# Optimization experiments

Measured on AMD Instinct MI355X. Metric: run time of the kernel, lower is better.

Reference implementation:

```python
import jax, jax.numpy as jnp
import numpy as np

T = 0.07
MOMENTUM = 0.5
B, D = 128, 128
N = 200000
K1 = 2048  # K + 1


def setup_inputs() -> dict:
    key = jax.random.key(0)
    ks = jax.random.split(key, 12)
    stdv = 1.0 / np.sqrt(D / 3.0)
    def bank(k):
        return jax.random.uniform(k, (N, D), dtype=jnp.float32) * (2 * stdv) - stdv
    l = jax.random.normal(ks[0], (B, D), dtype=jnp.float32)
    ab = jax.random.normal(ks[1], (B, D), dtype=jnp.float32)
    ori = jax.random.normal(ks[2], (B, D), dtype=jnp.float32)
    comp = jax.random.normal(ks[3], (B, D), dtype=jnp.float32)
    y = jax.random.randint(ks[4], (B,), 0, N, dtype=jnp.int32)
    idx = jax.random.randint(ks[5], (B, K1), 0, N, dtype=jnp.int32)
    idx = idx.at[:, 0].set(y)  # positive sample in slot 0
    return {
        'l': l, 'ab': ab, 'ori': ori, 'comp': comp, 'y': y, 'idx': idx,
        'memory_l': bank(ks[6]), 'memory_ab': bank(ks[7]),
        'memory_ori': bank(ks[8]), 'memory_comp': bank(ks[9]),
    }


def reference(l, ab, ori, comp, y, idx, memory_l, memory_ab, memory_ori, memory_comp):
    flat = idx.reshape(-1)
    # gather (B*K1, D) rows then fold back to (B, K1, D); weights are detached in torch
    w_l = jax.lax.stop_gradient(memory_l[flat]).reshape(B, K1, D)
    w_ab = jax.lax.stop_gradient(memory_ab[flat]).reshape(B, K1, D)
    w_ori = jax.lax.stop_gradient(memory_ori[flat]).reshape(B, K1, D)
    w_comp = jax.lax.stop_gradient(memory_comp[flat]).reshape(B, K1, D)

    dot = lambda w, v: jnp.einsum('bkd,bd->bk', w, v) / T  # use_softmax path
    out_ab_l = dot(w_l, ab)
    out_l_ori = dot(w_ori, l)
    out_ori_ab = dot(w_ab, ori)
    out_ab_comp = dot(w_comp, ab)
    out_l_comp = dot(w_comp, l)
    out_comp_ori = dot(w_ori, comp)
    outs = jnp.stack([out_l_ori, out_ab_l, out_ori_ab,
                      out_ab_comp, out_l_comp, out_comp_ori])[..., None]  # [6,B,K1,1]

    def ema_update(mem, v):
        pos = mem[y] * MOMENTUM + v * (1.0 - MOMENTUM)
        pos = pos / jnp.sqrt(jnp.sum(pos * pos, axis=1, keepdims=True))
        return mem.at[y].set(pos)

    return (outs,
            ema_update(memory_l, l),
            ema_update(memory_ab, ab),
            ema_update(memory_ori, ori),
            ema_update(memory_comp, comp))
```

## Files before the change

kernel.cpp:

```cpp
#include <hip/hip_runtime.h>

#define BB 128
#define DD 128
#define KK1 2048
#define NROWS 200000

static constexpr float INV_T = 1.0f / 0.07f;
static constexpr float MOM = 0.5f;

__global__ __launch_bounds__(256) void outs_kernel(
    const float* __restrict__ l, const float* __restrict__ ab,
    const float* __restrict__ ori, const float* __restrict__ comp,
    const int* __restrict__ idx,
    const float* __restrict__ ml, const float* __restrict__ mab,
    const float* __restrict__ mori, const float* __restrict__ mcomp,
    float* __restrict__ outs) {
  const int gid = blockIdx.x * blockDim.x + threadIdx.x;
  const int wave = gid >> 6;
  const int lane = threadIdx.x & 63;
  if (wave >= BB * KK1) return;
  const int b = wave >> 11;

  const int row = idx[wave];
  const size_t roff = (size_t)row * DD;

  const float2 wl    = ((const float2*)(ml    + roff))[lane];
  const float2 wab   = ((const float2*)(mab   + roff))[lane];
  const float2 wori  = ((const float2*)(mori  + roff))[lane];
  const float2 wcomp = ((const float2*)(mcomp + roff))[lane];

  const size_t voff = (size_t)b * DD;
  const float2 vl    = ((const float2*)(l    + voff))[lane];
  const float2 vab   = ((const float2*)(ab   + voff))[lane];
  const float2 vori  = ((const float2*)(ori  + voff))[lane];
  const float2 vcomp = ((const float2*)(comp + voff))[lane];

  float d0 = wori.x  * vl.x    + wori.y  * vl.y;
  float d1 = wl.x    * vab.x   + wl.y    * vab.y;
  float d2 = wab.x   * vori.x  + wab.y   * vori.y;
  float d3 = wcomp.x * vab.x   + wcomp.y * vab.y;
  float d4 = wcomp.x * vl.x    + wcomp.y * vl.y;
  float d5 = wori.x  * vcomp.x + wori.y  * vcomp.y;

#pragma unroll
  for (int off = 32; off > 0; off >>= 1) {
    d0 += __shfl_down(d0, off);
    d1 += __shfl_down(d1, off);
    d2 += __shfl_down(d2, off);
    d3 += __shfl_down(d3, off);
    d4 += __shfl_down(d4, off);
    d5 += __shfl_down(d5, off);
  }

  if (lane == 0) {
    const int BK = BB * KK1;
    outs[0 * BK + wave] = d0 * INV_T;
    outs[1 * BK + wave] = d1 * INV_T;
    outs[2 * BK + wave] = d2 * INV_T;
    outs[3 * BK + wave] = d3 * INV_T;
    outs[4 * BK + wave] = d4 * INV_T;
    outs[5 * BK + wave] = d5 * INV_T;
  }
}

__global__ __launch_bounds__(256) void copy_banks(
    const float4* __restrict__ s0, const float4* __restrict__ s1,
    const float4* __restrict__ s2, const float4* __restrict__ s3,
    float4* __restrict__ d0, float4* __restrict__ d1,
    float4* __restrict__ d2, float4* __restrict__ d3) {
  const int n = NROWS * DD / 4;
  const int stride = gridDim.x * blockDim.x;
  for (int i = blockIdx.x * blockDim.x + threadIdx.x; i < n; i += stride) {
    d0[i] = s0[i];
    d1[i] = s1[i];
    d2[i] = s2[i];
    d3[i] = s3[i];
  }
}

__global__ __launch_bounds__(64) void ema_kernel(
    const float* __restrict__ l, const float* __restrict__ ab,
    const float* __restrict__ ori, const float* __restrict__ comp,
    const int* __restrict__ y,
    const float* __restrict__ ml, const float* __restrict__ mab,
    const float* __restrict__ mori, const float* __restrict__ mcomp,
    float* __restrict__ ol, float* __restrict__ oab,
    float* __restrict__ oori, float* __restrict__ ocomp) {
  const int b = blockIdx.x;
  const int bank = blockIdx.y;
  const int row = y[b];
  for (int b2 = b + 1; b2 < BB; ++b2)
    if (y[b2] == row) return;

  const float* v;
  const float* mem;
  float* out;
  switch (bank) {
    case 0: v = l;    mem = ml;    out = ol;    break;
    case 1: v = ab;   mem = mab;   out = oab;   break;
    case 2: v = ori;  mem = mori;  out = oori;  break;
    default: v = comp; mem = mcomp; out = ocomp; break;
  }

  const int lane = threadIdx.x;
  const float2 m2 = ((const float2*)(mem + (size_t)row * DD))[lane];
  const float2 v2 = ((const float2*)(v + (size_t)b * DD))[lane];
  float2 p;
  p.x = m2.x * MOM + v2.x * (1.0f - MOM);
  p.y = m2.y * MOM + v2.y * (1.0f - MOM);

  float ss = p.x * p.x + p.y * p.y;
#pragma unroll
  for (int off = 32; off > 0; off >>= 1) ss += __shfl_down(ss, off);
  ss = __shfl(ss, 0);
  const float inv = 1.0f / sqrtf(ss);

  ((float2*)(out + (size_t)row * DD))[lane] = make_float2(p.x * inv, p.y * inv);
}

extern "C" void kernel_launch(void* const* d_in, const int* in_sizes, int n_in,
                              void* d_out, int out_size, void* d_ws, size_t ws_size,
                              hipStream_t stream) {
  const float* l     = (const float*)d_in[0];
  const float* ab    = (const float*)d_in[1];
  const float* ori   = (const float*)d_in[2];
  const float* comp  = (const float*)d_in[3];
  const int*   y     = (const int*)d_in[4];
  const int*   idx   = (const int*)d_in[5];
  const float* ml    = (const float*)d_in[6];
  const float* mab   = (const float*)d_in[7];
  const float* mori  = (const float*)d_in[8];
  const float* mcomp = (const float*)d_in[9];

  float* out = (float*)d_out;
  const size_t OUTS = (size_t)6 * BB * KK1;
  const size_t BANK = (size_t)NROWS * DD;
  float* o_outs  = out;
  float* o_ml    = out + OUTS;
  float* o_mab   = o_ml + BANK;
  float* o_mori  = o_mab + BANK;
  float* o_mcomp = o_mori + BANK;

  {
    const int waves = BB * KK1;
    const int blocks = waves / 4;
    outs_kernel<<<blocks, 256, 0, stream>>>(l, ab, ori, comp, idx,
                                            ml, mab, mori, mcomp, o_outs);
  }

  {
    copy_banks<<<4096, 256, 0, stream>>>(
        (const float4*)ml, (const float4*)mab, (const float4*)mori,
        (const float4*)mcomp, (float4*)o_ml, (float4*)o_mab,
        (float4*)o_mori, (float4*)o_mcomp);
  }

  {
    dim3 grid(BB, 4);
    ema_kernel<<<grid, 64, 0, stream>>>(l, ab, ori, comp, y,
                                        ml, mab, mori, mcomp,
                                        o_ml, o_mab, o_mori, o_mcomp);
  }
}
```

Before: 786.4 us.

## Fuse bank copy and gather-dot kernels into one interleaved launch

Merges the gather-dot kernel and the memory-bank copy kernel into a single launch. One of every five blocks does the bank copy and the other four compute the dot products, so the random-gather traffic and the streaming copy run at the same time instead of one after the other. The dot path now uses half-waves with float4 loads, two rows per wave, and xor shuffles over 32 lanes. The copy uses nontemporal stores to keep the output bank writes out of the cache. Interleaving the two kinds of block risks contention for bandwidth, and the block-index arithmetic must cover every row exactly.

```diff
diff --git a/kernel.cpp b/kernel.cpp
--- a/kernel.cpp
+++ b/kernel.cpp
@@ -8,73 +8,94 @@
 static constexpr float INV_T = 1.0f / 0.07f;
 static constexpr float MOM = 0.5f;
 
-__global__ __launch_bounds__(256) void outs_kernel(
+typedef float f4 __attribute__((ext_vector_type(4)));
+
+#define COPY_BLOCKS 8192
+#define OUTS_BLOCKS 32768
+#define TOTAL_BLOCKS (COPY_BLOCKS * 5)
+
+__global__ __launch_bounds__(256) void fused_kernel(
     const float* __restrict__ l, const float* __restrict__ ab,
     const float* __restrict__ ori, const float* __restrict__ comp,
     const int* __restrict__ idx,
     const float* __restrict__ ml, const float* __restrict__ mab,
     const float* __restrict__ mori, const float* __restrict__ mcomp,
-    float* __restrict__ outs) {
-  const int gid = blockIdx.x * blockDim.x + threadIdx.x;
-  const int wave = gid >> 6;
+    float* __restrict__ outs,
+    float* __restrict__ ol, float* __restrict__ oab,
+    float* __restrict__ oori, float* __restrict__ ocomp) {
+  const int bid = blockIdx.x;
+  const int q = bid / 5;
+  const int r = bid - q * 5;
+
+  if (r == 2) {
+    const int n = NROWS * DD / 4;
+    const int stride = COPY_BLOCKS * 256;
+    const f4* s0 = (const f4*)ml;
+    const f4* s1 = (const f4*)mab;
+    const f4* s2 = (const f4*)mori;
+    const f4* s3 = (const f4*)mcomp;
+    f4* d0 = (f4*)ol;
+    f4* d1 = (f4*)oab;
+    f4* d2 = (f4*)oori;
+    f4* d3 = (f4*)ocomp;
+    for (int i = q * 256 + threadIdx.x; i < n; i += stride) {
+      f4 a0 = s0[i];
+      f4 a1 = s1[i];
+      f4 a2 = s2[i];
+      f4 a3 = s3[i];
+      __builtin_nontemporal_store(a0, d0 + i);
+      __builtin_nontemporal_store(a1, d1 + i);
+      __builtin_nontemporal_store(a2, d2 + i);
+      __builtin_nontemporal_store(a3, d3 + i);
+    }
+    return;
+  }
+
+  const int ob = bid - q - (r > 2 ? 1 : 0);
   const int lane = threadIdx.x & 63;
-  if (wave >= BB * KK1) return;
-  const int b = wave >> 11;
+  const int hl = lane & 31;
+  const int w = ob * 8 + ((threadIdx.x >> 6) << 1) + (lane >> 5);
+  const int b = w >> 11;
 
-  const int row = idx[wave];
+  const int row = idx[w];
   const size_t roff = (size_t)row * DD;
 
-  const float2 wl    = ((const float2*)(ml    + roff))[lane];
-  const float2 wab   = ((const float2*)(mab   + roff))[lane];
-  const float2 wori  = ((const float2*)(mori  + roff))[lane];
-  const float2 wcomp = ((const float2*)(mcomp + roff))[lane];
+  const f4 wl    = ((const f4*)(ml    + roff))[hl];
+  const f4 wab   = ((const f4*)(mab   + roff))[hl];
+  const f4 wori  = ((const f4*)(mori  + roff))[hl];
+  const f4 wcomp = ((const f4*)(mcomp + roff))[hl];
 
   const size_t voff = (size_t)b * DD;
-  const float2 vl    = ((const float2*)(l    + voff))[lane];
-  const float2 vab   = ((const float2*)(ab   + voff))[lane];
-  const float2 vori  = ((const float2*)(ori  + voff))[lane];
-  const float2 vcomp = ((const float2*)(comp + voff))[lane];
+  const f4 vl    = ((const f4*)(l    + voff))[hl];
+  const f4 vab   = ((const f4*)(ab   + voff))[hl];
+  const f4 vori  = ((const f4*)(ori  + voff))[hl];
+  const f4 vcomp = ((const f4*)(comp + voff))[hl];
 
-  float d0 = wori.x  * vl.x    + wori.y  * vl.y;
-  float d1 = wl.x    * vab.x   + wl.y    * vab.y;
-  float d2 = wab.x   * vori.x  + wab.y   * vori.y;
-  float d3 = wcomp.x * vab.x   + wcomp.y * vab.y;
-  float d4 = wcomp.x * vl.x    + wcomp.y * vl.y;
-  float d5 = wori.x  * vcomp.x + wori.y  * vcomp.y;
+  float d0 = wori[0]*vl[0]    + wori[1]*vl[1]    + wori[2]*vl[2]    + wori[3]*vl[3];
+  float d1 = wl[0]*vab[0]     + wl[1]*vab[1]     + wl[2]*vab[2]     + wl[3]*vab[3];
+  float d2 = wab[0]*vori[0]   + wab[1]*vori[1]   + wab[2]*vori[2]   + wab[3]*vori[3];
+  float d3 = wcomp[0]*vab[0]  + wcomp[1]*vab[1]  + wcomp[2]*vab[2]  + wcomp[3]*vab[3];
+  float d4 = wcomp[0]*vl[0]   + wcomp[1]*vl[1]   + wcomp[2]*vl[2]   + wcomp[3]*vl[3];
+  float d5 = wori[0]*vcomp[0] + wori[1]*vcomp[1] + wori[2]*vcomp[2] + wori[3]*vcomp[3];
 
 #pragma unroll
-  for (int off = 32; off > 0; off >>= 1) {
-    d0 += __shfl_down(d0, off);
-    d1 += __shfl_down(d1, off);
-    d2 += __shfl_down(d2, off);
-    d3 += __shfl_down(d3, off);
-    d4 += __shfl_down(d4, off);
-    d5 += __shfl_down(d5, off);
+  for (int m = 16; m > 0; m >>= 1) {
+    d0 += __shfl_xor(d0, m);
+    d1 += __shfl_xor(d1, m);
+    d2 += __shfl_xor(d2, m);
+    d3 += __shfl_xor(d3, m);
+    d4 += __shfl_xor(d4, m);
+    d5 += __shfl_xor(d5, m);
   }
 
-  if (lane == 0) {
+  if (hl == 0) {
     const int BK = BB * KK1;
-    outs[0 * BK + wave] = d0 * INV_T;
-    outs[1 * BK + wave] = d1 * INV_T;
-    outs[2 * BK + wave] = d2 * INV_T;
-    outs[3 * BK + wave] = d3 * INV_T;
-    outs[4 * BK + wave] = d4 * INV_T;
-    outs[5 * BK + wave] = d5 * INV_T;
-  }
-}
-
-__global__ __launch_bounds__(256) void copy_banks(
-    const float4* __restrict__ s0, const float4* __restrict__ s1,
-    const float4* __restrict__ s2, const float4* __restrict__ s3,
-    float4* __restrict__ d0, float4* __restrict__ d1,
-    float4* __restrict__ d2, float4* __restrict__ d3) {
-  const int n = NROWS * DD / 4;
-  const int stride = gridDim.x * blockDim.x;
-  for (int i = blockIdx.x * blockDim.x + threadIdx.x; i < n; i += stride) {
-    d0[i] = s0[i];
-    d1[i] = s1[i];
-    d2[i] = s2[i];
-    d3[i] = s3[i];
+    outs[0 * BK + w] = d0 * INV_T;
+    outs[1 * BK + w] = d1 * INV_T;
+    outs[2 * BK + w] = d2 * INV_T;
+    outs[3 * BK + w] = d3 * INV_T;
+    outs[4 * BK + w] = d4 * INV_T;
+    outs[5 * BK + w] = d5 * INV_T;
   }
 }
 
@@ -141,19 +162,9 @@
   float* o_mori  = o_mab + BANK;
   float* o_mcomp = o_mori + BANK;
 
-  {
-    const int waves = BB * KK1;
-    const int blocks = waves / 4;
-    outs_kernel<<<blocks, 256, 0, stream>>>(l, ab, ori, comp, idx,
-                                            ml, mab, mori, mcomp, o_outs);
-  }
-
-  {
-    copy_banks<<<4096, 256, 0, stream>>>(
-        (const float4*)ml, (const float4*)mab, (const float4*)mori,
-        (const float4*)mcomp, (float4*)o_ml, (float4*)o_mab,
-        (float4*)o_mori, (float4*)o_mcomp);
-  }
+  fused_kernel<<<TOTAL_BLOCKS, 256, 0, stream>>>(
+      l, ab, ori, comp, idx, ml, mab, mori, mcomp,
+      o_outs, o_ml, o_mab, o_mori, o_mcomp);
 
   {
     dim3 grid(BB, 4);
```

Result: faster. 745.7 us (-5.2%).
